# Kernel tuning notes

Measured on AMD Instinct MI355X. Metric: run time of the kernel, lower is better.

Reference implementation:

```python
import jax, jax.numpy as jnp
import numpy as np

B, N, D0 = 128, 128, 512   # batch, n_objects, obj_dim
H, KD, R = 32, 64, 16      # n_heads, key_dim, n_relations
D = D0 + 1                 # with temporal tag

def setup_inputs() -> dict:
    key = jax.random.key(0)
    k1, k2, k3, k4, k5 = jax.random.split(key, 5)
    s = 0.02
    return {
        'obj_seq': jax.random.normal(k1, (B, N, D0), jnp.float32),
        'W_k':  jax.random.normal(k2, (KD, D), jnp.float32) * s,
        'W_q1': jax.random.normal(k3, (H * KD, D * N), jnp.float32) * s,
        'W_q2': jax.random.normal(k4, (H * KD, D * N), jnp.float32) * s,
        'W_s':  jax.random.normal(k5, (R, D), jnp.float32) * s,
    }

def reference(obj_seq, W_k, W_q1, W_q2, W_s):
    b, n, _ = obj_seq.shape
    # append temporal tag channel: obj -> [B, N, D]
    tag = jnp.broadcast_to(jnp.arange(n, dtype=obj_seq.dtype)[None, :, None], (b, n, 1))
    obj = jnp.concatenate([obj_seq, tag], axis=2)
    flat = obj.reshape(b, -1)                      # [B, N*D]
    Q1 = (flat @ W_q1.T).reshape(b, H, KD)         # [B, H, KD]
    Q2 = (flat @ W_q2.T).reshape(b, H, KD)
    K = obj @ W_k.T                                # [B, N, KD]
    # scores [B, N, H], softmax over objects (dim=1 in torch)
    A1 = jax.nn.softmax(jnp.einsum('bhk,bnk->bnh', Q1, K), axis=1)
    A2 = jax.nn.softmax(jnp.einsum('bhk,bnk->bnh', Q2, K), axis=1)
    # attention-weighted object sums: [B, H, D]
    E1 = jnp.einsum('bnh,bnd->bhd', A1, obj)
    E2 = jnp.einsum('bnh,bnd->bhd', A2, obj)
    Dr = E1 @ W_s.T - E2 @ W_s.T                   # [B, H, R]
    Dr = jnp.concatenate([Dr, E1[:, :, -1:], E2[:, :, -1:]], axis=2)  # [B, H, R+2]
    return Dr.reshape(b, -1)                       # [B, H*(R+2)]
```

## Files before the change

### kernel.cpp

```cpp
#include <hip/hip_runtime.h>
#include <cstdint>

typedef _Float16 f16;
typedef _Float16 f16x8 __attribute__((ext_vector_type(8)));
typedef float f32x4 __attribute__((ext_vector_type(4)));
typedef float floatx4 __attribute__((ext_vector_type(4)));

#define KTOT 65664
#define KSTEPS 2052
#define K64S 1026
#define DP 544

__device__ __forceinline__ void gload_lds16(const void* g, void* l) {
  __builtin_amdgcn_global_load_lds(
      (const __attribute__((address_space(1))) void*)g,
      (__attribute__((address_space(3))) void*)l, 16, 0, 0);
}

__global__ void prep_flat(const float* __restrict__ obj_seq, f16* __restrict__ flatKM) {
  int base = blockIdx.x * 1024 + threadIdx.x;
#pragma unroll
  for (int j = 0; j < 4; ++j) {
    int o = base + j * 256;
    int e = o & 7;
    int r = (o >> 3) & 127;
    int k8 = (o >> 10) & 3;
    int kb = o >> 12;
    int k = kb * 32 + k8 * 8 + e;
    int n = k / 513;
    int d = k - n * 513;
    float v = (d < 512) ? obj_seq[(((size_t)(r << 7) + n) << 9) + d] : (float)n;
    f16 h = (f16)v;
    size_t idx = (size_t)kb * 8192 + k8 * 1024 + r * 8 + e;
    flatKM[idx] = h;
    flatKM[idx + 4096] = (f16)(v - (float)h);
  }
}

__global__ void prep_obj(const float* __restrict__ obj_seq, f16* __restrict__ objHi,
                         f16* __restrict__ objLo, f16* __restrict__ objT16) {
  __shared__ f16 tile[32][132];
  int b = blockIdx.x / 17, c = blockIdx.x - 17 * (blockIdx.x / 17);
  int t = threadIdx.x;
  if (c < 16) {
#pragma unroll
    for (int i = 0; i < 16; ++i) {
      int e = t + i * 256;
      int n = e >> 5, dd = e & 31;
      float v = obj_seq[(((size_t)(b << 7) + n) << 9) + (c << 5) + dd];
      f16 h = (f16)v;
      objHi[((size_t)((b << 7) + n)) * DP + (c << 5) + dd] = h;
      objLo[((size_t)((b << 7) + n)) * DP + (c << 5) + dd] = (f16)(v - (float)h);
      tile[dd][n] = h;
    }
    __syncthreads();
#pragma unroll
    for (int i = 0; i < 16; ++i) {
      int e = t + i * 256;
      int dd = e >> 7, n = e & 127;
      objT16[(((size_t)b * DP + (c << 5) + dd) << 7) + n] = tile[dd][n];
    }
  } else {
#pragma unroll
    for (int i = 0; i < 16; ++i) {
      int e = t + i * 256;
      int n = e >> 5, dd = e & 31;
      f16 h = (dd == 0) ? (f16)(float)n : (f16)0.f;
      objHi[((size_t)((b << 7) + n)) * DP + 512 + dd] = h;
      objLo[((size_t)((b << 7) + n)) * DP + 512 + dd] = (f16)0.f;
    }
#pragma unroll
    for (int i = 0; i < 16; ++i) {
      int e = t + i * 256;
      int dd = e >> 7, n = e & 127;
      objT16[(((size_t)b * DP + 512 + dd) << 7) + n] = (dd == 0) ? (f16)(float)n : (f16)0.f;
    }
  }
}

__global__ void prep_wk(const float* __restrict__ W_k, f16* __restrict__ WkHi,
                        f16* __restrict__ WkLo) {
  int o = blockIdx.x * 256 + threadIdx.x;
  int kd = o / DP, d = o - kd * DP;
  float v = (d < 513) ? W_k[kd * 513 + d] * 1024.f : 0.f;
  f16 h = (f16)v;
  WkHi[o] = h;
  WkLo[o] = (f16)(v - (float)h);
}

__global__ __launch_bounds__(512, 2) void qgemm(const f16* __restrict__ flatKM,
                                                const float* __restrict__ Wq1,
                                                const float* __restrict__ Wq2,
                                                float* __restrict__ Qpart) {
  __shared__ __align__(16) char smem[131072];
  const int tid = threadIdx.x;
  const int lane = tid & 63;
  const int wave = tid >> 6;
  const int wm = wave >> 2, wn = wave & 3;
  const int l15 = lane & 15, lk = lane >> 4;
  const int ntile = blockIdx.x & 31;
  const int ksp = blockIdx.x >> 5;
  const int t0 = ksp * 129;
  const int nt = min(129, K64S - t0);
  const float* Wsrc = (ntile < 16) ? (Wq1 + (size_t)ntile * 128 * KTOT)
                                   : (Wq2 + (size_t)(ntile - 16) * 128 * KTOT);

  const float* wsrcs[4];
#pragma unroll
  for (int c = 0; c < 4; ++c) {
    int col = c * 32 + (tid >> 4);
    int chlog = (tid & 15) ^ (col & 15);
    wsrcs[c] = Wsrc + (size_t)col * KTOT + (size_t)t0 * 64 + chlog * 4;
  }
  const f16* asrc = flatKM + (size_t)t0 * 16384 + tid * 8;

  int aoff[2][4];
#pragma unroll
  for (int h = 0; h < 2; ++h)
#pragma unroll
    for (int mi = 0; mi < 4; ++mi)
      aoff[h][mi] = h * 16384 + lk * 2048 + (wm * 64 + mi * 16 + l15) * 16;
  int woff[2][2][2];
#pragma unroll
  for (int h = 0; h < 2; ++h)
#pragma unroll
    for (int nf = 0; nf < 2; ++nf) {
      int col = wn * 32 + nf * 16 + l15;
      int ch = h * 8 + lk * 2;
      woff[h][nf][0] = 32768 + col * 256 + ((ch) ^ l15) * 16;
      woff[h][nf][1] = 32768 + col * 256 + ((ch + 1) ^ l15) * 16;
    }

  f32x4 acc[4][2];
#pragma unroll
  for (int mi = 0; mi < 4; ++mi)
#pragma unroll
    for (int nf = 0; nf < 2; ++nf) acc[mi][nf] = (f32x4){0.f, 0.f, 0.f, 0.f};

  auto stage = [&](int tt) {
    char* S = smem + (tt & 1) * 65536;
#pragma unroll
    for (int c = 0; c < 4; ++c)
      gload_lds16(asrc + (size_t)tt * 16384 + c * 4096, S + c * 8192 + tid * 16);
#pragma unroll
    for (int c = 0; c < 4; ++c)
      gload_lds16(wsrcs[c] + (size_t)tt * 64, S + 32768 + c * 8192 + tid * 16);
  };

  stage(0);
  stage(1);

  for (int t = 0; t < nt; ++t) {
    if (t < nt - 1) asm volatile("s_waitcnt vmcnt(8)" ::: "memory");
    else            asm volatile("s_waitcnt vmcnt(0)" ::: "memory");
    __builtin_amdgcn_s_barrier();
    __builtin_amdgcn_sched_barrier(0);
    const char* S = smem + (t & 1) * 65536;

#pragma unroll
    for (int h = 0; h < 2; ++h) {
      f16x8 afh[4], afl[4];
#pragma unroll
      for (int mi = 0; mi < 4; ++mi) {
        afh[mi] = *(const f16x8*)(S + aoff[h][mi]);
        afl[mi] = *(const f16x8*)(S + aoff[h][mi] + 8192);
      }
      floatx4 wv[2][2];
#pragma unroll
      for (int nf = 0; nf < 2; ++nf) {
        wv[nf][0] = *(const floatx4*)(S + woff[h][nf][0]);
        wv[nf][1] = *(const floatx4*)(S + woff[h][nf][1]);
      }
      f16x8 whi[2], wlo[2];
#pragma unroll
      for (int nf = 0; nf < 2; ++nf)
#pragma unroll
        for (int j = 0; j < 4; ++j) {
          { float v = wv[nf][0][j] * 1024.f; f16 hh = (f16)v; whi[nf][j] = hh; wlo[nf][j] = (f16)(v - (float)hh); }
          { float v = wv[nf][1][j] * 1024.f; f16 hh = (f16)v; whi[nf][4 + j] = hh; wlo[nf][4 + j] = (f16)(v - (float)hh); }
        }
#pragma unroll
      for (int mi = 0; mi < 4; ++mi)
#pragma unroll
        for (int nf = 0; nf < 2; ++nf) {
          acc[mi][nf] = __builtin_amdgcn_mfma_f32_16x16x32_f16(afh[mi], whi[nf], acc[mi][nf], 0, 0, 0);
          acc[mi][nf] = __builtin_amdgcn_mfma_f32_16x16x32_f16(afh[mi], wlo[nf], acc[mi][nf], 0, 0, 0);
          acc[mi][nf] = __builtin_amdgcn_mfma_f32_16x16x32_f16(afl[mi], whi[nf], acc[mi][nf], 0, 0, 0);
        }
    }

    __builtin_amdgcn_sched_barrier(0);
    __builtin_amdgcn_s_barrier();
    if (t + 2 < nt) stage(t + 2);
  }

  const float s = 1.f / 1024.f;
  float* qout = Qpart + (size_t)ksp * 524288;
#pragma unroll
  for (int mi = 0; mi < 4; ++mi) {
    int row = wm * 64 + mi * 16 + lk * 4;
#pragma unroll
    for (int nf = 0; nf < 2; ++nf) {
      int col = ntile * 128 + wn * 32 + nf * 16 + l15;
#pragma unroll
      for (int j = 0; j < 4; ++j)
        qout[(size_t)(row + j) * 4096 + col] = acc[mi][nf][j] * s;
    }
  }
}

__global__ __launch_bounds__(512, 1) void predinet_tail(
    const f16* __restrict__ objHi, const f16* __restrict__ objLo, const f16* __restrict__ objT16,
    const f16* __restrict__ WkHi, const f16* __restrict__ WkLo,
    const float* __restrict__ Qpart, const float* __restrict__ W_s, float* __restrict__ out) {
  __shared__ __align__(16) char smem[105984];
  const int b = blockIdx.x;
  const int tid = threadIdx.x, lane = tid & 63, wave = tid >> 6;
  const int l15 = lane & 15, lk = lane >> 4;

  f16* WT = (f16*)(smem);
  f16* Qh = (f16*)(smem + 17408);
  f16* Ql = (f16*)(smem + 26624);
  f16* Kh = (f16*)(smem + 35840);
  f16* Kl = (f16*)(smem + 54272);
  float* S = (float*)(smem + 72704);
  f16* E = (f16*)(smem + 17408);
  float* DL = (float*)(smem + 96832);

  {
    const float* qp = Qpart + (size_t)b * 4096 + tid * 8;
    floatx4 q0 = (floatx4){0.f, 0.f, 0.f, 0.f};
    floatx4 q1 = (floatx4){0.f, 0.f, 0.f, 0.f};
#pragma unroll
    for (int p = 0; p < 8; ++p) {
      q0 += *(const floatx4*)(qp + (size_t)p * 524288);
      q1 += *(const floatx4*)(qp + (size_t)p * 524288 + 4);
    }
    int hp = tid >> 3, kd = (tid * 8) & 63;
    f16x8 vh, vl;
#pragma unroll
    for (int j = 0; j < 4; ++j) {
      f16 h0 = (f16)q0[j]; vh[j] = h0; vl[j] = (f16)(q0[j] - (float)h0);
      f16 h1 = (f16)q1[j]; vh[4 + j] = h1; vl[4 + j] = (f16)(q1[j] - (float)h1);
    }
    *(f16x8*)(Qh + hp * 72 + kd) = vh;
    *(f16x8*)(Ql + hp * 72 + kd) = vl;
  }
  {
    f32x4 acc[4];
#pragma unroll
    for (int nf = 0; nf < 4; ++nf) acc[nf] = (f32x4){0.f, 0.f, 0.f, 0.f};
    const f16* arowH = objHi + ((size_t)(b * 128) + wave * 16 + l15) * DP + lk * 8;
    const f16* arowL = objLo + ((size_t)(b * 128) + wave * 16 + l15) * DP + lk * 8;
    const f16* bhi = WkHi + (size_t)l15 * DP + lk * 8;
    const f16* blo = WkLo + (size_t)l15 * DP + lk * 8;
    for (int ks = 0; ks < 17; ++ks) {
      f16x8 ah = *(const f16x8*)(arowH + ks * 32);
      f16x8 al = *(const f16x8*)(arowL + ks * 32);
#pragma unroll
      for (int nf = 0; nf < 4; ++nf) {
        f16x8 h = *(const f16x8*)(bhi + (size_t)nf * 16 * DP + ks * 32);
        f16x8 l = *(const f16x8*)(blo + (size_t)nf * 16 * DP + ks * 32);
        acc[nf] = __builtin_amdgcn_mfma_f32_16x16x32_f16(ah, h, acc[nf], 0, 0, 0);
        acc[nf] = __builtin_amdgcn_mfma_f32_16x16x32_f16(ah, l, acc[nf], 0, 0, 0);
        acc[nf] = __builtin_amdgcn_mfma_f32_16x16x32_f16(al, h, acc[nf], 0, 0, 0);
      }
    }
#pragma unroll
    for (int nf = 0; nf < 4; ++nf)
#pragma unroll
      for (int j = 0; j < 4; ++j) {
        float kv = acc[nf][j] * (1.f / 1024.f);
        f16 h = (f16)kv;
        Kh[(wave * 16 + lk * 4 + j) * 72 + nf * 16 + l15] = h;
        Kl[(wave * 16 + lk * 4 + j) * 72 + nf * 16 + l15] = (f16)(kv - (float)h);
      }
  }
  __syncthreads();
  {
    f32x4 acc[4];
#pragma unroll
    for (int nf = 0; nf < 4; ++nf) acc[nf] = (f32x4){0.f, 0.f, 0.f, 0.f};
#pragma unroll
    for (int ks = 0; ks < 2; ++ks) {
      f16x8 ah = *(const f16x8*)(Kh + (wave * 16 + l15) * 72 + ks * 32 + lk * 8);
      f16x8 al = *(const f16x8*)(Kl + (wave * 16 + l15) * 72 + ks * 32 + lk * 8);
#pragma unroll
      for (int nf = 0; nf < 4; ++nf) {
        f16x8 bh = *(const f16x8*)(Qh + (nf * 16 + l15) * 72 + ks * 32 + lk * 8);
        f16x8 bl = *(const f16x8*)(Ql + (nf * 16 + l15) * 72 + ks * 32 + lk * 8);
        acc[nf] = __builtin_amdgcn_mfma_f32_16x16x32_f16(ah, bh, acc[nf], 0, 0, 0);
        acc[nf] = __builtin_amdgcn_mfma_f32_16x16x32_f16(ah, bl, acc[nf], 0, 0, 0);
        acc[nf] = __builtin_amdgcn_mfma_f32_16x16x32_f16(al, bh, acc[nf], 0, 0, 0);
      }
    }
#pragma unroll
    for (int nf = 0; nf < 4; ++nf)
#pragma unroll
      for (int j = 0; j < 4; ++j)
        S[(wave * 16 + lk * 4 + j) * 65 + nf * 16 + l15] = acc[nf][j];
  }
  __syncthreads();
  {
#pragma unroll
    for (int ci = 0; ci < 8; ++ci) {
      int c = wave * 8 + ci;
      float s0 = S[lane * 65 + c], s1 = S[(lane + 64) * 65 + c];
      float m = fmaxf(s0, s1);
      for (int off = 32; off; off >>= 1) m = fmaxf(m, __shfl_xor(m, off));
      float e0 = __expf(s0 - m), e1 = __expf(s1 - m);
      float sum = e0 + e1;
      for (int off = 32; off; off >>= 1) sum += __shfl_xor(sum, off);
      float inv = 1.f / sum;
      WT[c * 136 + lane] = (f16)(e0 * inv);
      WT[c * 136 + 64 + lane] = (f16)(e1 * inv);
    }
  }
  __syncthreads();
  {
    f16x8 bw[4][4];
#pragma unroll
    for (int nf = 0; nf < 4; ++nf)
#pragma unroll
      for (int ks = 0; ks < 4; ++ks)
        bw[nf][ks] = *(const f16x8*)(WT + (nf * 16 + l15) * 136 + ks * 32 + lk * 8);
    for (int r = 0; r < 5; ++r) {
      int mi = r * 8 + wave;
      if (mi >= 34) break;
      const f16* arow = objT16 + (((size_t)b * DP + mi * 16 + l15) << 7) + lk * 8;
      f16x8 a[4];
#pragma unroll
      for (int ks = 0; ks < 4; ++ks) a[ks] = *(const f16x8*)(arow + ks * 32);
#pragma unroll
      for (int nf = 0; nf < 4; ++nf) {
        f32x4 acc = (f32x4){0.f, 0.f, 0.f, 0.f};
#pragma unroll
        for (int ks = 0; ks < 4; ++ks)
          acc = __builtin_amdgcn_mfma_f32_16x16x32_f16(a[ks], bw[nf][ks], acc, 0, 0, 0);
#pragma unroll
        for (int j = 0; j < 4; ++j)
          E[(mi * 16 + lk * 4 + j) * 73 + nf * 16 + l15] = (f16)acc[j];
      }
    }
  }
  __syncthreads();
  {
    f16* Ws16 = WT;
    for (int i = tid; i < 16 * DP; i += 512) {
      int r = i / DP, d = i - r * DP;
      Ws16[i] = (f16)((d < 513) ? W_s[r * 513 + d] : 0.f);
    }
  }
  __syncthreads();
  if (wave < 4) {
    const f16* Ws16 = WT;
    f32x4 acc = (f32x4){0.f, 0.f, 0.f, 0.f};
    for (int ks = 0; ks < 17; ++ks) {
      f16x8 a = *(const f16x8*)(Ws16 + l15 * DP + ks * 32 + lk * 8);
      f16x8 bv;
#pragma unroll
      for (int jj = 0; jj < 8; ++jj)
        bv[jj] = E[(ks * 32 + lk * 8 + jj) * 73 + wave * 16 + l15];
      acc = __builtin_amdgcn_mfma_f32_16x16x32_f16(a, bv, acc, 0, 0, 0);
    }
#pragma unroll
    for (int j = 0; j < 4; ++j) DL[(lk * 4 + j) * 64 + wave * 16 + l15] = acc[j];
  }
  __syncthreads();
  {
    int h = tid >> 4, r = tid & 15;
    float v = DL[r * 64 + h] - DL[r * 64 + 32 + h];
    out[(size_t)b * 576 + h * 18 + r] = v;
    if (tid < 64) {
      int set = tid >> 5, hh = tid & 31;
      out[(size_t)b * 576 + hh * 18 + 16 + set] = (float)E[512 * 73 + set * 32 + hh];
    }
  }
}

extern "C" void kernel_launch(void* const* d_in, const int* in_sizes, int n_in,
                              void* d_out, int out_size, void* d_ws, size_t ws_size,
                              hipStream_t stream) {
  const float* obj_seq = (const float*)d_in[0];
  const float* W_k = (const float*)d_in[1];
  const float* W_q1 = (const float*)d_in[2];
  const float* W_q2 = (const float*)d_in[3];
  const float* W_s = (const float*)d_in[4];
  float* out = (float*)d_out;

  char* ws = (char*)d_ws;
  size_t off = 0;
  auto carve = [&](size_t bytes) -> char* {
    char* p = ws + off;
    off += (bytes + 255) & ~(size_t)255;
    return p;
  };
  f16* flatKM = (f16*)carve((size_t)KSTEPS * 8192 * 2);
  f16* objHi = (f16*)carve((size_t)16384 * DP * 2);
  f16* objLo = (f16*)carve((size_t)16384 * DP * 2);
  f16* objT16 = (f16*)carve((size_t)128 * DP * 128 * 2);
  f16* WkHi = (f16*)carve((size_t)64 * DP * 2);
  f16* WkLo = (f16*)carve((size_t)64 * DP * 2);
  float* Qpart = (float*)carve((size_t)8 * 524288 * 4);
  (void)ws_size; (void)in_sizes; (void)n_in; (void)out_size;

  prep_flat<<<8208, 256, 0, stream>>>(obj_seq, flatKM);
  prep_obj<<<2176, 256, 0, stream>>>(obj_seq, objHi, objLo, objT16);
  prep_wk<<<136, 256, 0, stream>>>(W_k, WkHi, WkLo);
  qgemm<<<256, 512, 0, stream>>>(flatKM, W_q1, W_q2, Qpart);
  predinet_tail<<<128, 512, 0, stream>>>(objHi, objLo, objT16, WkHi, WkLo, Qpart, W_s, out);
}
```

Baseline: 379.2 us.

## Restructure Q GEMM with bf16 split, register-staged weights and doubled split-K

Switches the split-precision Q projection from fp16 hi/lo with 1024x scaling to bf16 hi/lo obtained by bit truncation, which drops the scaling step. The A operand is now read straight from global into registers in an MFMA-ready layout, and the weights are prefetched into registers, split and stored to a small swizzled LDS buffer once per tile. This removes the per-wave repeated fp32->f16 conversion and shrinks LDS from 128KB to 32KB to allow more resident blocks. The K dimension is split into 16 partitions instead of 8, so the tail kernel sums twice as many partial buffers and twice the Qpart memory traffic is paid. Accuracy may change because bf16 hi/lo carries fewer mantissa bits than fp16 hi/lo.

```diff
diff --git a/kernel.cpp b/kernel.cpp
--- a/kernel.cpp
+++ b/kernel.cpp
@@ -3,38 +3,46 @@
 
 typedef _Float16 f16;
 typedef _Float16 f16x8 __attribute__((ext_vector_type(8)));
+typedef short s16x8 __attribute__((ext_vector_type(8)));
+typedef unsigned u32x4 __attribute__((ext_vector_type(4)));
 typedef float f32x4 __attribute__((ext_vector_type(4)));
 typedef float floatx4 __attribute__((ext_vector_type(4)));
 
 #define KTOT 65664
 #define KSTEPS 2052
-#define K64S 1026
 #define DP 544
 
-__device__ __forceinline__ void gload_lds16(const void* g, void* l) {
-  __builtin_amdgcn_global_load_lds(
-      (const __attribute__((address_space(1))) void*)g,
-      (__attribute__((address_space(3))) void*)l, 16, 0, 0);
-}
-
-__global__ void prep_flat(const float* __restrict__ obj_seq, f16* __restrict__ flatKM) {
-  int base = blockIdx.x * 1024 + threadIdx.x;
-#pragma unroll
-  for (int j = 0; j < 4; ++j) {
-    int o = base + j * 256;
-    int e = o & 7;
-    int r = (o >> 3) & 127;
-    int k8 = (o >> 10) & 3;
-    int kb = o >> 12;
-    int k = kb * 32 + k8 * 8 + e;
-    int n = k / 513;
-    int d = k - n * 513;
-    float v = (d < 512) ? obj_seq[(((size_t)(r << 7) + n) << 9) + d] : (float)n;
-    f16 h = (f16)v;
-    size_t idx = (size_t)kb * 8192 + k8 * 1024 + r * 8 + e;
-    flatKM[idx] = h;
-    flatKM[idx + 4096] = (f16)(v - (float)h);
-  }
+__device__ __forceinline__ unsigned bfpack(float e0, float e1) {
+  return (__float_as_uint(e0) >> 16) | (__float_as_uint(e1) & 0xffff0000u);
+}
+__device__ __forceinline__ float bfhi(float x) {
+  return __uint_as_float(__float_as_uint(x) & 0xffff0000u);
+}
+
+__global__ void prep_flat(const float* __restrict__ obj_seq, char* __restrict__ flatA) {
+  int o = blockIdx.x * 256 + threadIdx.x;
+  int g = o & 3;
+  int row = (o >> 2) & 127;
+  int pl = (o >> 9) & 1;
+  int kb = o >> 10;
+  int k0 = kb * 32 + g * 8;
+  unsigned w[4];
+#pragma unroll
+  for (int j = 0; j < 8; j += 2) {
+    float v[2];
+#pragma unroll
+    for (int jj = 0; jj < 2; ++jj) {
+      int k = k0 + j + jj;
+      int n = k / 513;
+      int d = k - n * 513;
+      float x = (d < 512) ? obj_seq[(((size_t)(row << 7) + n) << 9) + d] : (float)n;
+      if (pl) x = x - bfhi(x);
+      v[jj] = x;
+    }
+    w[j >> 1] = bfpack(v[0], v[1]);
+  }
+  *(u32x4*)(flatA + (size_t)kb * 16384 + pl * 8192 + row * 64 + g * 16) =
+      (u32x4){w[0], w[1], w[2], w[3]};
 }
 
 __global__ void prep_obj(const float* __restrict__ obj_seq, f16* __restrict__ objHi,
@@ -88,123 +96,131 @@
   WkLo[o] = (f16)(v - (float)h);
 }
 
-__global__ __launch_bounds__(512, 2) void qgemm(const f16* __restrict__ flatKM,
+__global__ __launch_bounds__(512, 4) void qgemm(const char* __restrict__ flatA,
                                                 const float* __restrict__ Wq1,
                                                 const float* __restrict__ Wq2,
                                                 float* __restrict__ Qpart) {
-  __shared__ __align__(16) char smem[131072];
+  __shared__ __align__(16) char smem[32768];
   const int tid = threadIdx.x;
   const int lane = tid & 63;
   const int wave = tid >> 6;
-  const int wm = wave >> 2, wn = wave & 3;
+  const int wm = wave >> 1, wn = wave & 1;
   const int l15 = lane & 15, lk = lane >> 4;
   const int ntile = blockIdx.x & 31;
   const int ksp = blockIdx.x >> 5;
   const int t0 = ksp * 129;
-  const int nt = min(129, K64S - t0);
+  const int nt = min(129, KSTEPS - t0);
   const float* Wsrc = (ntile < 16) ? (Wq1 + (size_t)ntile * 128 * KTOT)
                                    : (Wq2 + (size_t)(ntile - 16) * 128 * KTOT);
 
-  const float* wsrcs[4];
-#pragma unroll
-  for (int c = 0; c < 4; ++c) {
-    int col = c * 32 + (tid >> 4);
-    int chlog = (tid & 15) ^ (col & 15);
-    wsrcs[c] = Wsrc + (size_t)col * KTOT + (size_t)t0 * 64 + chlog * 4;
-  }
-  const f16* asrc = flatKM + (size_t)t0 * 16384 + tid * 8;
-
-  int aoff[2][4];
-#pragma unroll
-  for (int h = 0; h < 2; ++h)
-#pragma unroll
-    for (int mi = 0; mi < 4; ++mi)
-      aoff[h][mi] = h * 16384 + lk * 2048 + (wm * 64 + mi * 16 + l15) * 16;
-  int woff[2][2][2];
-#pragma unroll
-  for (int h = 0; h < 2; ++h)
-#pragma unroll
-    for (int nf = 0; nf < 2; ++nf) {
-      int col = wn * 32 + nf * 16 + l15;
-      int ch = h * 8 + lk * 2;
-      woff[h][nf][0] = 32768 + col * 256 + ((ch) ^ l15) * 16;
-      woff[h][nf][1] = 32768 + col * 256 + ((ch + 1) ^ l15) * 16;
-    }
-
-  f32x4 acc[4][2];
-#pragma unroll
-  for (int mi = 0; mi < 4; ++mi)
-#pragma unroll
-    for (int nf = 0; nf < 2; ++nf) acc[mi][nf] = (f32x4){0.f, 0.f, 0.f, 0.f};
-
-  auto stage = [&](int tt) {
-    char* S = smem + (tt & 1) * 65536;
-#pragma unroll
-    for (int c = 0; c < 4; ++c)
-      gload_lds16(asrc + (size_t)tt * 16384 + c * 4096, S + c * 8192 + tid * 16);
-#pragma unroll
-    for (int c = 0; c < 4; ++c)
-      gload_lds16(wsrcs[c] + (size_t)tt * 64, S + 32768 + c * 8192 + tid * 16);
+  const int wc = tid >> 2, wgr = tid & 3;
+  const float* wg = Wsrc + (size_t)wc * KTOT + (size_t)t0 * 32 + wgr * 8;
+  const int wwr = wc * 64 + (wgr ^ (wc & 3)) * 16;
+  int wrd[4];
+#pragma unroll
+  for (int nf = 0; nf < 4; ++nf) {
+    int col = wn * 64 + nf * 16 + l15;
+    wrd[nf] = col * 64 + (lk ^ (col & 3)) * 16;
+  }
+  int aoff[2];
+#pragma unroll
+  for (int mi = 0; mi < 2; ++mi) aoff[mi] = (wm * 32 + mi * 16 + l15) * 64 + lk * 16;
+  const char* aBase = flatA;
+
+  f32x4 acc[2][4];
+#pragma unroll
+  for (int mi = 0; mi < 2; ++mi)
+#pragma unroll
+    for (int nf = 0; nf < 4; ++nf) acc[mi][nf] = (f32x4){0.f, 0.f, 0.f, 0.f};
+
+  char* slot0 = smem;
+  char* slot1 = smem + 16384;
+
+  auto WSTORE = [&](char* dst, floatx4 (&wr)[2]) {
+    u32x4 HV = (u32x4){bfpack(wr[0][0], wr[0][1]), bfpack(wr[0][2], wr[0][3]),
+                       bfpack(wr[1][0], wr[1][1]), bfpack(wr[1][2], wr[1][3])};
+    float l0 = wr[0][0] - bfhi(wr[0][0]), l1 = wr[0][1] - bfhi(wr[0][1]);
+    float l2 = wr[0][2] - bfhi(wr[0][2]), l3 = wr[0][3] - bfhi(wr[0][3]);
+    float l4 = wr[1][0] - bfhi(wr[1][0]), l5 = wr[1][1] - bfhi(wr[1][1]);
+    float l6 = wr[1][2] - bfhi(wr[1][2]), l7 = wr[1][3] - bfhi(wr[1][3]);
+    u32x4 LV = (u32x4){bfpack(l0, l1), bfpack(l2, l3), bfpack(l4, l5), bfpack(l6, l7)};
+    *(u32x4*)(dst + wwr) = HV;
+    *(u32x4*)(dst + wwr + 8192) = LV;
   };
-
-  stage(0);
-  stage(1);
-
-  for (int t = 0; t < nt; ++t) {
-    if (t < nt - 1) asm volatile("s_waitcnt vmcnt(8)" ::: "memory");
-    else            asm volatile("s_waitcnt vmcnt(0)" ::: "memory");
+  auto ALOAD = [&](int tt, s16x8 (&aH)[2], s16x8 (&aL)[2]) {
+    const char* ab = aBase + (size_t)(t0 + tt) * 16384;
+#pragma unroll
+    for (int mi = 0; mi < 2; ++mi) {
+      aH[mi] = *(const s16x8*)(ab + aoff[mi]);
+      aL[mi] = *(const s16x8*)(ab + 8192 + aoff[mi]);
+    }
+  };
+
+  auto STEP = [&](int t, const char* cur, char* nxt,
+                  s16x8 (&aHc)[2], s16x8 (&aLc)[2],
+                  s16x8 (&aHn)[2], s16x8 (&aLn)[2],
+                  floatx4 (&wrN)[2], floatx4 (&wrF)[2]) {
+    const bool h1 = (t + 1 < nt), h2 = (t + 2 < nt);
+    if (h1) WSTORE(nxt, wrN);
+    if (h2) {
+      wrF[0] = *(const floatx4*)(wg + (size_t)(t + 2) * 32);
+      wrF[1] = *(const floatx4*)(wg + (size_t)(t + 2) * 32 + 4);
+    }
+    if (h1) ALOAD(t + 1, aHn, aLn);
+#pragma unroll
+    for (int np = 0; np < 2; ++np) {
+      s16x8 wH[2], wL[2];
+#pragma unroll
+      for (int q = 0; q < 2; ++q) {
+        wH[q] = *(const s16x8*)(cur + wrd[np * 2 + q]);
+        wL[q] = *(const s16x8*)(cur + wrd[np * 2 + q] + 8192);
+      }
+#pragma unroll
+      for (int mi = 0; mi < 2; ++mi)
+#pragma unroll
+        for (int q = 0; q < 2; ++q) {
+          int nf = np * 2 + q;
+          acc[mi][nf] = __builtin_amdgcn_mfma_f32_16x16x32_bf16(aHc[mi], wH[q], acc[mi][nf], 0, 0, 0);
+          acc[mi][nf] = __builtin_amdgcn_mfma_f32_16x16x32_bf16(aHc[mi], wL[q], acc[mi][nf], 0, 0, 0);
+          acc[mi][nf] = __builtin_amdgcn_mfma_f32_16x16x32_bf16(aLc[mi], wH[q], acc[mi][nf], 0, 0, 0);
+        }
+    }
+    asm volatile("s_waitcnt lgkmcnt(0)" ::: "memory");
+    __builtin_amdgcn_sched_barrier(0);
     __builtin_amdgcn_s_barrier();
     __builtin_amdgcn_sched_barrier(0);
-    const char* S = smem + (t & 1) * 65536;
-
-#pragma unroll
-    for (int h = 0; h < 2; ++h) {
-      f16x8 afh[4], afl[4];
-#pragma unroll
-      for (int mi = 0; mi < 4; ++mi) {
-        afh[mi] = *(const f16x8*)(S + aoff[h][mi]);
-        afl[mi] = *(const f16x8*)(S + aoff[h][mi] + 8192);
-      }
-      floatx4 wv[2][2];
-#pragma unroll
-      for (int nf = 0; nf < 2; ++nf) {
-        wv[nf][0] = *(const floatx4*)(S + woff[h][nf][0]);
-        wv[nf][1] = *(const floatx4*)(S + woff[h][nf][1]);
-      }
-      f16x8 whi[2], wlo[2];
-#pragma unroll
-      for (int nf = 0; nf < 2; ++nf)
-#pragma unroll
-        for (int j = 0; j < 4; ++j) {
-          { float v = wv[nf][0][j] * 1024.f; f16 hh = (f16)v; whi[nf][j] = hh; wlo[nf][j] = (f16)(v - (float)hh); }
-          { float v = wv[nf][1][j] * 1024.f; f16 hh = (f16)v; whi[nf][4 + j] = hh; wlo[nf][4 + j] = (f16)(v - (float)hh); }
-        }
-#pragma unroll
-      for (int mi = 0; mi < 4; ++mi)
-#pragma unroll
-        for (int nf = 0; nf < 2; ++nf) {
-          acc[mi][nf] = __builtin_amdgcn_mfma_f32_16x16x32_f16(afh[mi], whi[nf], acc[mi][nf], 0, 0, 0);
-          acc[mi][nf] = __builtin_amdgcn_mfma_f32_16x16x32_f16(afh[mi], wlo[nf], acc[mi][nf], 0, 0, 0);
-          acc[mi][nf] = __builtin_amdgcn_mfma_f32_16x16x32_f16(afl[mi], whi[nf], acc[mi][nf], 0, 0, 0);
-        }
-    }
-
-    __builtin_amdgcn_sched_barrier(0);
-    __builtin_amdgcn_s_barrier();
-    if (t + 2 < nt) stage(t + 2);
-  }
-
-  const float s = 1.f / 1024.f;
+  };
+
+  s16x8 aH0[2], aL0[2], aH1[2], aL1[2];
+  floatx4 wr0[2], wr1[2];
+  wr0[0] = *(const floatx4*)(wg);
+  wr0[1] = *(const floatx4*)(wg + 4);
+  ALOAD(0, aH0, aL0);
+  wr1[0] = *(const floatx4*)(wg + 32);
+  wr1[1] = *(const floatx4*)(wg + 36);
+  WSTORE(slot0, wr0);
+  asm volatile("s_waitcnt lgkmcnt(0)" ::: "memory");
+  __builtin_amdgcn_s_barrier();
+  __builtin_amdgcn_sched_barrier(0);
+
+  int t = 0;
+  while (true) {
+    STEP(t, slot0, slot1, aH0, aL0, aH1, aL1, wr1, wr0);
+    if (++t >= nt) break;
+    STEP(t, slot1, slot0, aH1, aL1, aH0, aL0, wr0, wr1);
+    if (++t >= nt) break;
+  }
+
   float* qout = Qpart + (size_t)ksp * 524288;
 #pragma unroll
-  for (int mi = 0; mi < 4; ++mi) {
-    int row = wm * 64 + mi * 16 + lk * 4;
-#pragma unroll
-    for (int nf = 0; nf < 2; ++nf) {
-      int col = ntile * 128 + wn * 32 + nf * 16 + l15;
+  for (int mi = 0; mi < 2; ++mi) {
+    int row = wm * 32 + mi * 16 + lk * 4;
+#pragma unroll
+    for (int nf = 0; nf < 4; ++nf) {
+      int col = ntile * 128 + wn * 64 + nf * 16 + l15;
 #pragma unroll
       for (int j = 0; j < 4; ++j)
-        qout[(size_t)(row + j) * 4096 + col] = acc[mi][nf][j] * s;
+        qout[(size_t)(row + j) * 4096 + col] = acc[mi][nf][j];
     }
   }
 }
@@ -232,7 +248,7 @@
     floatx4 q0 = (floatx4){0.f, 0.f, 0.f, 0.f};
     floatx4 q1 = (floatx4){0.f, 0.f, 0.f, 0.f};
 #pragma unroll
-    for (int p = 0; p < 8; ++p) {
+    for (int p = 0; p < 16; ++p) {
       q0 += *(const floatx4*)(qp + (size_t)p * 524288);
       q1 += *(const floatx4*)(qp + (size_t)p * 524288 + 4);
     }
@@ -395,18 +411,18 @@
     off += (bytes + 255) & ~(size_t)255;
     return p;
   };
-  f16* flatKM = (f16*)carve((size_t)KSTEPS * 8192 * 2);
+  char* flatA = carve((size_t)KSTEPS * 16384);
   f16* objHi = (f16*)carve((size_t)16384 * DP * 2);
   f16* objLo = (f16*)carve((size_t)16384 * DP * 2);
   f16* objT16 = (f16*)carve((size_t)128 * DP * 128 * 2);
   f16* WkHi = (f16*)carve((size_t)64 * DP * 2);
   f16* WkLo = (f16*)carve((size_t)64 * DP * 2);
-  float* Qpart = (float*)carve((size_t)8 * 524288 * 4);
+  float* Qpart = (float*)carve((size_t)16 * 524288 * 4);
   (void)ws_size; (void)in_sizes; (void)n_in; (void)out_size;
 
-  prep_flat<<<8208, 256, 0, stream>>>(obj_seq, flatKM);
+  prep_flat<<<8208, 256, 0, stream>>>(obj_seq, flatA);
   prep_obj<<<2176, 256, 0, stream>>>(obj_seq, objHi, objLo, objT16);
   prep_wk<<<136, 256, 0, stream>>>(W_k, WkHi, WkLo);
-  qgemm<<<256, 512, 0, stream>>>(flatKM, W_q1, W_q2, Qpart);
+  qgemm<<<512, 512, 0, stream>>>(flatA, W_q1, W_q2, Qpart);
   predinet_tail<<<128, 512, 0, stream>>>(objHi, objLo, objT16, WkHi, WkLo, Qpart, W_s, out);
 }
```

Measured after the change: 453.2 us. 19.5% more time.

## Switch Q GEMM to bf16 hi/lo split with smaller K stages and more blocks

Applied to the files above, without the earlier changes.

Replaces the fp16 hi/lo split (with 1024x scaling) in the big Q projection GEMM by a bf16 split done with bit masking. Each K stage shrinks from 64 to 32, halving the LDS footprint so four blocks of 512 threads can reside per CU. The grid doubles to 512 blocks with a 16-way K split, and the tail kernel now sums 16 partial Q buffers. The intent is more latency hiding and cheaper weight conversion. The cost is twice as many barrier round-trips per block, more partial-sum traffic in the tail, and a small accuracy risk from bf16's 8-bit mantissa in the hi/lo split.

```diff
diff --git a/kernel.cpp b/kernel.cpp
--- a/kernel.cpp
+++ b/kernel.cpp
@@ -3,12 +3,13 @@
 
 typedef _Float16 f16;
 typedef _Float16 f16x8 __attribute__((ext_vector_type(8)));
+typedef short s16x8 __attribute__((ext_vector_type(8)));
+typedef unsigned u32x4 __attribute__((ext_vector_type(4)));
 typedef float f32x4 __attribute__((ext_vector_type(4)));
 typedef float floatx4 __attribute__((ext_vector_type(4)));
 
 #define KTOT 65664
 #define KSTEPS 2052
-#define K64S 1026
 #define DP 544
 
 __device__ __forceinline__ void gload_lds16(const void* g, void* l) {
@@ -17,24 +18,36 @@
       (__attribute__((address_space(3))) void*)l, 16, 0, 0);
 }
 
-__global__ void prep_flat(const float* __restrict__ obj_seq, f16* __restrict__ flatKM) {
-  int base = blockIdx.x * 1024 + threadIdx.x;
-#pragma unroll
-  for (int j = 0; j < 4; ++j) {
-    int o = base + j * 256;
-    int e = o & 7;
-    int r = (o >> 3) & 127;
-    int k8 = (o >> 10) & 3;
-    int kb = o >> 12;
-    int k = kb * 32 + k8 * 8 + e;
-    int n = k / 513;
-    int d = k - n * 513;
-    float v = (d < 512) ? obj_seq[(((size_t)(r << 7) + n) << 9) + d] : (float)n;
-    f16 h = (f16)v;
-    size_t idx = (size_t)kb * 8192 + k8 * 1024 + r * 8 + e;
-    flatKM[idx] = h;
-    flatKM[idx + 4096] = (f16)(v - (float)h);
-  }
+__device__ __forceinline__ unsigned bfpack(float e0, float e1) {
+  return (__float_as_uint(e0) >> 16) | (__float_as_uint(e1) & 0xffff0000u);
+}
+__device__ __forceinline__ float bfhi(float x) {
+  return __uint_as_float(__float_as_uint(x) & 0xffff0000u);
+}
+
+__global__ void prep_flat(const float* __restrict__ obj_seq, char* __restrict__ flatA) {
+  int o = blockIdx.x * 256 + threadIdx.x;
+  int row = o & 127;
+  int k8 = (o >> 7) & 3;
+  int pl = (o >> 9) & 1;
+  int kb = o >> 10;
+  int k0 = kb * 32 + k8 * 8;
+  unsigned w[4];
+#pragma unroll
+  for (int j = 0; j < 8; j += 2) {
+    float v[2];
+#pragma unroll
+    for (int jj = 0; jj < 2; ++jj) {
+      int k = k0 + j + jj;
+      int n = k / 513;
+      int d = k - n * 513;
+      float x = (d < 512) ? obj_seq[(((size_t)(row << 7) + n) << 9) + d] : (float)n;
+      if (pl) x = x - bfhi(x);
+      v[jj] = x;
+    }
+    w[j >> 1] = bfpack(v[0], v[1]);
+  }
+  *(u32x4*)(flatA + (size_t)o * 16) = (u32x4){w[0], w[1], w[2], w[3]};
 }
 
 __global__ void prep_obj(const float* __restrict__ obj_seq, f16* __restrict__ objHi,
@@ -88,11 +101,11 @@
   WkLo[o] = (f16)(v - (float)h);
 }
 
-__global__ __launch_bounds__(512, 2) void qgemm(const f16* __restrict__ flatKM,
+__global__ __launch_bounds__(512, 4) void qgemm(const char* __restrict__ flatA,
                                                 const float* __restrict__ Wq1,
                                                 const float* __restrict__ Wq2,
                                                 float* __restrict__ Qpart) {
-  __shared__ __align__(16) char smem[131072];
+  __shared__ __align__(16) char smem[65536];
   const int tid = threadIdx.x;
   const int lane = tid & 63;
   const int wave = tid >> 6;
@@ -101,100 +114,91 @@
   const int ntile = blockIdx.x & 31;
   const int ksp = blockIdx.x >> 5;
   const int t0 = ksp * 129;
-  const int nt = min(129, K64S - t0);
+  const int nt = min(129, KSTEPS - t0);
   const float* Wsrc = (ntile < 16) ? (Wq1 + (size_t)ntile * 128 * KTOT)
                                    : (Wq2 + (size_t)(ntile - 16) * 128 * KTOT);
 
-  const float* wsrcs[4];
-#pragma unroll
-  for (int c = 0; c < 4; ++c) {
-    int col = c * 32 + (tid >> 4);
-    int chlog = (tid & 15) ^ (col & 15);
-    wsrcs[c] = Wsrc + (size_t)col * KTOT + (size_t)t0 * 64 + chlog * 4;
-  }
-  const f16* asrc = flatKM + (size_t)t0 * 16384 + tid * 8;
+  const char* asrc = flatA + (size_t)t0 * 16384 + tid * 16;
+  const float* wsrc0;
+  const float* wsrc1;
+  {
+    int c0 = (tid >> 3), c1 = 64 + (tid >> 3);
+    wsrc0 = Wsrc + (size_t)c0 * KTOT + (size_t)t0 * 32 + (((tid & 7) ^ (c0 & 7)) << 2);
+    wsrc1 = Wsrc + (size_t)c1 * KTOT + (size_t)t0 * 32 + (((tid & 7) ^ (c1 & 7)) << 2);
+  }
 
   int aoff[2][4];
 #pragma unroll
-  for (int h = 0; h < 2; ++h)
+  for (int pl = 0; pl < 2; ++pl)
 #pragma unroll
     for (int mi = 0; mi < 4; ++mi)
-      aoff[h][mi] = h * 16384 + lk * 2048 + (wm * 64 + mi * 16 + l15) * 16;
-  int woff[2][2][2];
-#pragma unroll
-  for (int h = 0; h < 2; ++h)
+      aoff[pl][mi] = pl * 8192 + lk * 2048 + (wm * 64 + mi * 16 + l15) * 16;
+  int woff[2][2];
+#pragma unroll
+  for (int nf = 0; nf < 2; ++nf) {
+    int col = wn * 32 + nf * 16 + l15;
+#pragma unroll
+    for (int j = 0; j < 2; ++j)
+      woff[nf][j] = 16384 + col * 128 + (((2 * lk + j) ^ (col & 7)) << 4);
+  }
+
+  f32x4 acc[4][2];
+#pragma unroll
+  for (int mi = 0; mi < 4; ++mi)
+#pragma unroll
+    for (int nf = 0; nf < 2; ++nf) acc[mi][nf] = (f32x4){0.f, 0.f, 0.f, 0.f};
+
+  auto stage = [&](int tt) {
+    char* S = smem + (tt & 1) * 32768;
+    gload_lds16(asrc + (size_t)tt * 16384, S + tid * 16);
+    gload_lds16(asrc + (size_t)tt * 16384 + 8192, S + 8192 + tid * 16);
+    gload_lds16(wsrc0 + (size_t)tt * 32, S + 16384 + tid * 16);
+    gload_lds16(wsrc1 + (size_t)tt * 32, S + 24576 + tid * 16);
+  };
+
+  auto compute = [&](const char* S) {
+    s16x8 wH[2], wL[2];
 #pragma unroll
     for (int nf = 0; nf < 2; ++nf) {
-      int col = wn * 32 + nf * 16 + l15;
-      int ch = h * 8 + lk * 2;
-      woff[h][nf][0] = 32768 + col * 256 + ((ch) ^ l15) * 16;
-      woff[h][nf][1] = 32768 + col * 256 + ((ch + 1) ^ l15) * 16;
-    }
-
-  f32x4 acc[4][2];
-#pragma unroll
-  for (int mi = 0; mi < 4; ++mi)
-#pragma unroll
-    for (int nf = 0; nf < 2; ++nf) acc[mi][nf] = (f32x4){0.f, 0.f, 0.f, 0.f};
-
-  auto stage = [&](int tt) {
-    char* S = smem + (tt & 1) * 65536;
-#pragma unroll
-    for (int c = 0; c < 4; ++c)
-      gload_lds16(asrc + (size_t)tt * 16384 + c * 4096, S + c * 8192 + tid * 16);
-#pragma unroll
-    for (int c = 0; c < 4; ++c)
-      gload_lds16(wsrcs[c] + (size_t)tt * 64, S + 32768 + c * 8192 + tid * 16);
+      floatx4 a = *(const floatx4*)(S + woff[nf][0]);
+      floatx4 b = *(const floatx4*)(S + woff[nf][1]);
+      u32x4 H = (u32x4){bfpack(a[0], a[1]), bfpack(a[2], a[3]),
+                        bfpack(b[0], b[1]), bfpack(b[2], b[3])};
+      float l0 = a[0] - bfhi(a[0]), l1 = a[1] - bfhi(a[1]);
+      float l2 = a[2] - bfhi(a[2]), l3 = a[3] - bfhi(a[3]);
+      float l4 = b[0] - bfhi(b[0]), l5 = b[1] - bfhi(b[1]);
+      float l6 = b[2] - bfhi(b[2]), l7 = b[3] - bfhi(b[3]);
+      u32x4 L = (u32x4){bfpack(l0, l1), bfpack(l2, l3), bfpack(l4, l5), bfpack(l6, l7)};
+      wH[nf] = *(s16x8*)&H;
+      wL[nf] = *(s16x8*)&L;
+    }
+#pragma unroll
+    for (int mi = 0; mi < 4; ++mi) {
+      s16x8 aH = *(const s16x8*)(S + aoff[0][mi]);
+      s16x8 aL = *(const s16x8*)(S + aoff[1][mi]);
+#pragma unroll
+      for (int nf = 0; nf < 2; ++nf) {
+        acc[mi][nf] = __builtin_amdgcn_mfma_f32_16x16x32_bf16(aH, wH[nf], acc[mi][nf], 0, 0, 0);
+        acc[mi][nf] = __builtin_amdgcn_mfma_f32_16x16x32_bf16(aH, wL[nf], acc[mi][nf], 0, 0, 0);
+        acc[mi][nf] = __builtin_amdgcn_mfma_f32_16x16x32_bf16(aL, wH[nf], acc[mi][nf], 0, 0, 0);
+      }
+    }
   };
 
   stage(0);
   stage(1);
 
   for (int t = 0; t < nt; ++t) {
-    if (t < nt - 1) asm volatile("s_waitcnt vmcnt(8)" ::: "memory");
+    if (t < nt - 1) asm volatile("s_waitcnt vmcnt(4)" ::: "memory");
     else            asm volatile("s_waitcnt vmcnt(0)" ::: "memory");
     __builtin_amdgcn_s_barrier();
     __builtin_amdgcn_sched_barrier(0);
-    const char* S = smem + (t & 1) * 65536;
-
-#pragma unroll
-    for (int h = 0; h < 2; ++h) {
-      f16x8 afh[4], afl[4];
-#pragma unroll
-      for (int mi = 0; mi < 4; ++mi) {
-        afh[mi] = *(const f16x8*)(S + aoff[h][mi]);
-        afl[mi] = *(const f16x8*)(S + aoff[h][mi] + 8192);
-      }
-      floatx4 wv[2][2];
-#pragma unroll
-      for (int nf = 0; nf < 2; ++nf) {
-        wv[nf][0] = *(const floatx4*)(S + woff[h][nf][0]);
-        wv[nf][1] = *(const floatx4*)(S + woff[h][nf][1]);
-      }
-      f16x8 whi[2], wlo[2];
-#pragma unroll
-      for (int nf = 0; nf < 2; ++nf)
-#pragma unroll
-        for (int j = 0; j < 4; ++j) {
-          { float v = wv[nf][0][j] * 1024.f; f16 hh = (f16)v; whi[nf][j] = hh; wlo[nf][j] = (f16)(v - (float)hh); }
-          { float v = wv[nf][1][j] * 1024.f; f16 hh = (f16)v; whi[nf][4 + j] = hh; wlo[nf][4 + j] = (f16)(v - (float)hh); }
-        }
-#pragma unroll
-      for (int mi = 0; mi < 4; ++mi)
-#pragma unroll
-        for (int nf = 0; nf < 2; ++nf) {
-          acc[mi][nf] = __builtin_amdgcn_mfma_f32_16x16x32_f16(afh[mi], whi[nf], acc[mi][nf], 0, 0, 0);
-          acc[mi][nf] = __builtin_amdgcn_mfma_f32_16x16x32_f16(afh[mi], wlo[nf], acc[mi][nf], 0, 0, 0);
-          acc[mi][nf] = __builtin_amdgcn_mfma_f32_16x16x32_f16(afl[mi], whi[nf], acc[mi][nf], 0, 0, 0);
-        }
-    }
-
+    compute(smem + (t & 1) * 32768);
     __builtin_amdgcn_sched_barrier(0);
     __builtin_amdgcn_s_barrier();
     if (t + 2 < nt) stage(t + 2);
   }
 
-  const float s = 1.f / 1024.f;
   float* qout = Qpart + (size_t)ksp * 524288;
 #pragma unroll
   for (int mi = 0; mi < 4; ++mi) {
@@ -204,7 +208,7 @@
       int col = ntile * 128 + wn * 32 + nf * 16 + l15;
 #pragma unroll
       for (int j = 0; j < 4; ++j)
-        qout[(size_t)(row + j) * 4096 + col] = acc[mi][nf][j] * s;
+        qout[(size_t)(row + j) * 4096 + col] = acc[mi][nf][j];
     }
   }
 }
@@ -232,7 +236,7 @@
     floatx4 q0 = (floatx4){0.f, 0.f, 0.f, 0.f};
     floatx4 q1 = (floatx4){0.f, 0.f, 0.f, 0.f};
 #pragma unroll
-    for (int p = 0; p < 8; ++p) {
+    for (int p = 0; p < 16; ++p) {
       q0 += *(const floatx4*)(qp + (size_t)p * 524288);
       q1 += *(const floatx4*)(qp + (size_t)p * 524288 + 4);
     }
@@ -395,18 +399,18 @@
     off += (bytes + 255) & ~(size_t)255;
     return p;
   };
-  f16* flatKM = (f16*)carve((size_t)KSTEPS * 8192 * 2);
+  char* flatA = carve((size_t)KSTEPS * 16384);
   f16* objHi = (f16*)carve((size_t)16384 * DP * 2);
   f16* objLo = (f16*)carve((size_t)16384 * DP * 2);
   f16* objT16 = (f16*)carve((size_t)128 * DP * 128 * 2);
   f16* WkHi = (f16*)carve((size_t)64 * DP * 2);
   f16* WkLo = (f16*)carve((size_t)64 * DP * 2);
-  float* Qpart = (float*)carve((size_t)8 * 524288 * 4);
+  float* Qpart = (float*)carve((size_t)16 * 524288 * 4);
   (void)ws_size; (void)in_sizes; (void)n_in; (void)out_size;
 
-  prep_flat<<<8208, 256, 0, stream>>>(obj_seq, flatKM);
+  prep_flat<<<8208, 256, 0, stream>>>(obj_seq, flatA);
   prep_obj<<<2176, 256, 0, stream>>>(obj_seq, objHi, objLo, objT16);
   prep_wk<<<136, 256, 0, stream>>>(W_k, WkHi, WkLo);
-  qgemm<<<256, 512, 0, stream>>>(flatKM, W_q1, W_q2, Qpart);
+  qgemm<<<512, 512, 0, stream>>>(flatA, W_q1, W_q2, Qpart);
   predinet_tail<<<128, 512, 0, stream>>>(objHi, objLo, objT16, WkHi, WkLo, Qpart, W_s, out);
 }
```

Result: faster. 366.8 us (-3.3%).
